# Kernel tuning notes

Measured on AMD Instinct MI355X. Metric: run time of the kernel, lower is better.

The kernel has to match this reference:

```python
import jax, jax.numpy as jnp
import numpy as np

C, T, H, W, K = 12, 10, 4, 7, 3  # hardcoded in the original forward
PAD = 1
EPS = 1e-5


def setup_inputs() -> dict:
    key = jax.random.key(0)
    ks = jax.random.split(key, 14)
    nt = 32768
    x = jax.random.normal(ks[0], (nt, C, T, H * W), jnp.float32)
    # G: Linear(T -> 2T) -> BN1d(2T) -> ReLU -> Linear(2T -> K) -> Softmax
    w_g1 = jax.random.normal(ks[1], (2 * T, T), jnp.float32) * 0.3
    g1_gamma = 1.0 + 0.1 * jax.random.normal(ks[2], (2 * T,), jnp.float32)
    g1_beta = 0.1 * jax.random.normal(ks[3], (2 * T,), jnp.float32)
    g1_mean = 0.1 * jax.random.normal(ks[4], (2 * T,), jnp.float32)
    g1_var = jax.random.uniform(ks[5], (2 * T,), jnp.float32, 0.5, 1.5)
    w_g2 = jax.random.normal(ks[6], (K, 2 * T), jnp.float32) * 0.3
    # L: Conv1d(C -> C//4, K) -> BN1d(C//4) -> ReLU -> Conv1d(C//4 -> C, 1) -> Sigmoid
    w_l1 = jax.random.normal(ks[7], (C // 4, C, K), jnp.float32) * 0.3
    l1_gamma = 1.0 + 0.1 * jax.random.normal(ks[8], (C // 4,), jnp.float32)
    l1_beta = 0.1 * jax.random.normal(ks[9], (C // 4,), jnp.float32)
    l1_mean = 0.1 * jax.random.normal(ks[10], (C // 4,), jnp.float32)
    l1_var = jax.random.uniform(ks[11], (C // 4,), jnp.float32, 0.5, 1.5)
    w_l2 = jax.random.normal(ks[12], (C, C // 4, 1), jnp.float32) * 0.3
    return dict(x=x, w_g1=w_g1, g1_gamma=g1_gamma, g1_beta=g1_beta,
                g1_mean=g1_mean, g1_var=g1_var, w_g2=w_g2, w_l1=w_l1,
                l1_gamma=l1_gamma, l1_beta=l1_beta, l1_mean=l1_mean,
                l1_var=l1_var, w_l2=w_l2)


def reference(x, w_g1, g1_gamma, g1_beta, g1_mean, g1_var, w_g2,
              w_l1, l1_gamma, l1_beta, l1_mean, l1_var, w_l2):
    n = x.shape[0]
    new_x = x.reshape(n, C, T, H, W)
    # adaptive_avg_pool2d((1,1)) == mean over spatial dims -> [n, C, T]
    pooled = new_x.mean(axis=(3, 4))
    # --- G branch: per-(sample,channel) temporal kernel, [n, C, K] ---
    rows = pooled.reshape(n * C, T)
    z = rows @ w_g1.T
    z = (z - g1_mean) * jax.lax.rsqrt(g1_var + EPS) * g1_gamma + g1_beta
    z = jax.nn.relu(z)
    kern = jax.nn.softmax(z @ w_g2.T, axis=-1).reshape(n, C, K)
    # --- L branch: local channel-temporal gating, [n, C, T] ---
    a = jax.lax.conv_general_dilated(pooled, w_l1, (1,), [(K // 2, K // 2)],
                                     dimension_numbers=('NCH', 'OIH', 'NCH'))
    a = (a - l1_mean[None, :, None]) * jax.lax.rsqrt(l1_var + EPS)[None, :, None] \
        * l1_gamma[None, :, None] + l1_beta[None, :, None]
    a = jax.nn.relu(a)
    a = jax.lax.conv_general_dilated(a, w_l2, (1,), [(0, 0)],
                                     dimension_numbers=('NCH', 'OIH', 'NCH'))
    act = jax.nn.sigmoid(a)  # [n, C, T]
    # --- modulate and apply per-(sample,channel) depthwise temporal conv ---
    xm = new_x * act[:, :, :, None, None]  # [n, C, T, H, W]
    xp = jnp.pad(xm, ((0, 0), (0, 0), (PAD, PAD), (0, 0), (0, 0)))
    out = kern[:, :, 0, None, None, None] * xp[:, :, 0:T]
    for j in range(1, K):  # K=3, tiny structural loop
        out = out + kern[:, :, j, None, None, None] * xp[:, :, j:j + T]
    # permute [n,c,t,h,w] -> [n,t,c,h,w] and flatten time into batch
    out = jnp.transpose(out, (0, 2, 1, 3, 4)).reshape(n * T, C, H, W)
    return out
```

## Files before the change

kernel.cpp:

```cpp
#include <hip/hip_runtime.h>


#define CC 12
#define TT 10
#define SAMPLE 3360
#define SAMPLE4 840
#define EPSF 1e-5f

typedef float f4 __attribute__((ext_vector_type(4)));

__global__ __launch_bounds__(128) void tam_kernel(
    const float* __restrict__ x,
    const float* __restrict__ w_g1,
    const float* __restrict__ g1_gamma, const float* __restrict__ g1_beta,
    const float* __restrict__ g1_mean,  const float* __restrict__ g1_var,
    const float* __restrict__ w_g2,
    const float* __restrict__ w_l1,
    const float* __restrict__ l1_gamma, const float* __restrict__ l1_beta,
    const float* __restrict__ l1_mean,  const float* __restrict__ l1_var,
    const float* __restrict__ w_l2,
    float* __restrict__ out)
{
    __shared__ f4    sx4[SAMPLE4];
    __shared__ float spool[120];
    __shared__ float sz[240];
    __shared__ float sa1[30];
    __shared__ float skern[36];

    const int n    = blockIdx.x;
    const int tid  = threadIdx.x;
    const int wid  = tid >> 6;
    const int lane = tid & 63;

    const f4* xg = reinterpret_cast<const f4*>(x + (size_t)n * SAMPLE);
    for (int i = wid; i < 13; i += 2) {
        __builtin_amdgcn_global_load_lds(
            (const __attribute__((address_space(1))) void*)(xg + i * 64 + lane),
            (__attribute__((address_space(3))) void*)(&sx4[i * 64]),
            16, 0, 0);
    }
    if (tid < 8) sx4[832 + tid] = xg[832 + tid];
    __syncthreads();

    if (tid < 120) {
        const f4* rp = sx4 + tid * 7;
        f4 a = rp[0];
        #pragma unroll
        for (int i = 1; i < 7; ++i) a += rp[i];
        spool[tid] = (a.x + a.y + a.z + a.w) * (1.0f / 28.0f);
    }
    __syncthreads();

    for (int task = tid; task < 270; task += 128) {
        if (task < 240) {
            const int c = task / 20, j = task % 20;
            float s = 0.f;
            #pragma unroll
            for (int t = 0; t < TT; ++t)
                s += spool[c * TT + t] * w_g1[j * TT + t];
            const float rs = rsqrtf(g1_var[j] + EPSF);
            sz[task] = fmaxf((s - g1_mean[j]) * rs * g1_gamma[j] + g1_beta[j], 0.f);
        } else {
            const int e = task - 240;
            const int m = e / TT, t = e % TT;
            float s = 0.f;
            #pragma unroll
            for (int c = 0; c < CC; ++c) {
                #pragma unroll
                for (int k = 0; k < 3; ++k) {
                    const int t2 = t + k - 1;
                    if (t2 >= 0 && t2 < TT)
                        s += spool[c * TT + t2] * w_l1[(m * CC + c) * 3 + k];
                }
            }
            const float rs = rsqrtf(l1_var[m] + EPSF);
            sa1[e] = fmaxf((s - l1_mean[m]) * rs * l1_gamma[m] + l1_beta[m], 0.f);
        }
    }
    __syncthreads();

    float* sact = spool;
    if (tid >= 116) {
        const int c = tid - 116;
        float sc0 = 0.f, sc1 = 0.f, sc2 = 0.f;
        #pragma unroll
        for (int j = 0; j < 20; ++j) {
            const float zj = sz[c * 20 + j];
            sc0 += zj * w_g2[j];
            sc1 += zj * w_g2[20 + j];
            sc2 += zj * w_g2[40 + j];
        }
        const float mx = fmaxf(sc0, fmaxf(sc1, sc2));
        const float e0 = __expf(sc0 - mx), e1 = __expf(sc1 - mx), e2 = __expf(sc2 - mx);
        const float ri = 1.0f / (e0 + e1 + e2);
        skern[c]      = e0 * ri;
        skern[12 + c] = e1 * ri;
        skern[24 + c] = e2 * ri;
    }
    if (tid < 120) {
        const int c = tid / TT, t = tid % TT;
        float s = 0.f;
        #pragma unroll
        for (int m = 0; m < 3; ++m) s += sa1[m * TT + t] * w_l2[c * 3 + m];
        sact[tid] = 1.0f / (1.0f + __expf(-s));
    }
    __syncthreads();

    f4* og = reinterpret_cast<f4*>(out + (size_t)n * SAMPLE);
    #pragma unroll
    for (int k = 0; k < 7; ++k) {
        const int v = tid + k * 128;
        if (k < 6 || tid < 72) {
            const int t   = v / 84;
            const int rem = v % 84;
            const int c   = rem / 7;
            const int s4  = rem % 7;
            const int base = c * 70 + s4;
            const float k0 = skern[c];
            const float k1 = skern[12 + c];
            const float k2 = skern[24 + c];
            f4 acc = (k1 * sact[c * TT + t]) * sx4[base + t * 7];
            if (t > 0)
                acc += (k0 * sact[c * TT + t - 1]) * sx4[base + (t - 1) * 7];
            if (t < TT - 1)
                acc += (k2 * sact[c * TT + t + 1]) * sx4[base + (t + 1) * 7];
            __builtin_nontemporal_store(acc, og + v);
        }
    }
}

extern "C" void kernel_launch(void* const* d_in, const int* in_sizes, int n_in,
                              void* d_out, int out_size, void* d_ws, size_t ws_size,
                              hipStream_t stream) {
    (void)n_in; (void)out_size; (void)d_ws; (void)ws_size;
    const float* x        = (const float*)d_in[0];
    const float* w_g1     = (const float*)d_in[1];
    const float* g1_gamma = (const float*)d_in[2];
    const float* g1_beta  = (const float*)d_in[3];
    const float* g1_mean  = (const float*)d_in[4];
    const float* g1_var   = (const float*)d_in[5];
    const float* w_g2     = (const float*)d_in[6];
    const float* w_l1     = (const float*)d_in[7];
    const float* l1_gamma = (const float*)d_in[8];
    const float* l1_beta  = (const float*)d_in[9];
    const float* l1_mean  = (const float*)d_in[10];
    const float* l1_var   = (const float*)d_in[11];
    const float* w_l2     = (const float*)d_in[12];
    float* out = (float*)d_out;

    const int n_total = in_sizes[0] / SAMPLE;
    tam_kernel<<<n_total, 128, 0, stream>>>(
        x, w_g1, g1_gamma, g1_beta, g1_mean, g1_var, w_g2,
        w_l1, l1_gamma, l1_beta, l1_mean, l1_var, w_l2, out);
}
```

Before: 193.6 us.

## Process two samples per 256-thread block with lightweight LDS barriers

Each block now loads two samples into separate LDS buffers up front with async global-to-LDS loads, then processes them sequentially with 256 threads. Syncs inside the per-sample pipeline are replaced by s_barrier plus an explicit lgkmcnt wait and sched barriers. The aim is to amortize block launch and barrier overhead and to keep more loads in flight per block. LDS per block doubles, which may reduce occupancy, and the second sample's load no longer overlaps with other blocks' compute. The grid assumes an even sample count.

```diff
diff --git a/kernel.cpp b/kernel.cpp
--- a/kernel.cpp
+++ b/kernel.cpp
@@ -9,7 +9,106 @@
 
 typedef float f4 __attribute__((ext_vector_type(4)));
 
-__global__ __launch_bounds__(128) void tam_kernel(
+#define FENCE() __builtin_amdgcn_sched_barrier(0)
+#define BLOCK_SYNC() do { asm volatile("s_waitcnt lgkmcnt(0)" ::: "memory"); \
+    FENCE(); __builtin_amdgcn_s_barrier(); FENCE(); } while (0)
+
+
+__device__ __forceinline__ void process_sample(
+    const f4* __restrict__ sx4, float* __restrict__ p,
+    const float* __restrict__ w_g1,
+    const float* __restrict__ g1_gamma, const float* __restrict__ g1_beta,
+    const float* __restrict__ g1_mean,  const float* __restrict__ g1_var,
+    const float* __restrict__ w_g2,
+    const float* __restrict__ w_l1,
+    const float* __restrict__ l1_gamma, const float* __restrict__ l1_beta,
+    const float* __restrict__ l1_mean,  const float* __restrict__ l1_var,
+    const float* __restrict__ w_l2,
+    f4* __restrict__ og, int tid)
+{
+    if (tid < 120) {
+        const f4* rp = sx4 + tid * 7;
+        f4 a = rp[0];
+        #pragma unroll
+        for (int i = 1; i < 7; ++i) a += rp[i];
+        p[tid] = (a.x + a.y + a.z + a.w) * (1.0f / 28.0f);
+    }
+    BLOCK_SYNC();
+
+    for (int task = tid; task < 270; task += 256) {
+        if (task < 240) {
+            const int c = task / 20, j = task % 20;
+            float s = 0.f;
+            #pragma unroll
+            for (int t = 0; t < TT; ++t)
+                s += p[c * TT + t] * w_g1[j * TT + t];
+            const float rs = rsqrtf(g1_var[j] + EPSF);
+            p[120 + task] = fmaxf((s - g1_mean[j]) * rs * g1_gamma[j] + g1_beta[j], 0.f);
+        } else {
+            const int e = task - 240;
+            const int m = e / TT, t = e % TT;
+            float s = 0.f;
+            #pragma unroll
+            for (int c = 0; c < CC; ++c) {
+                #pragma unroll
+                for (int k = 0; k < 3; ++k) {
+                    const int t2 = t + k - 1;
+                    if (t2 >= 0 && t2 < TT)
+                        s += p[c * TT + t2] * w_l1[(m * CC + c) * 3 + k];
+                }
+            }
+            const float rs = rsqrtf(l1_var[m] + EPSF);
+            p[360 + e] = fmaxf((s - l1_mean[m]) * rs * l1_gamma[m] + l1_beta[m], 0.f);
+        }
+    }
+    BLOCK_SYNC();
+
+    if (tid < CC) {
+        const int c = tid;
+        float sc0 = 0.f, sc1 = 0.f, sc2 = 0.f;
+        #pragma unroll
+        for (int j = 0; j < 20; ++j) {
+            const float zj = p[120 + c * 20 + j];
+            sc0 += zj * w_g2[j];
+            sc1 += zj * w_g2[20 + j];
+            sc2 += zj * w_g2[40 + j];
+        }
+        const float mx = fmaxf(sc0, fmaxf(sc1, sc2));
+        const float e0 = __expf(sc0 - mx), e1 = __expf(sc1 - mx), e2 = __expf(sc2 - mx);
+        const float ri = 1.0f / (e0 + e1 + e2);
+        p[390 + c] = e0 * ri;
+        p[402 + c] = e1 * ri;
+        p[414 + c] = e2 * ri;
+    }
+    if (tid >= 64 && tid < 64 + 120) {
+        const int idx = tid - 64;
+        const int c = idx / TT, t = idx % TT;
+        float s = 0.f;
+        #pragma unroll
+        for (int m = 0; m < 3; ++m) s += p[360 + m * TT + t] * w_l2[c * 3 + m];
+        p[idx] = 1.0f / (1.0f + __expf(-s));
+    }
+    BLOCK_SYNC();
+
+    for (int v = tid; v < SAMPLE4; v += 256) {
+        const int t   = v / 84;
+        const int rem = v % 84;
+        const int c   = rem / 7;
+        const int s4  = rem % 7;
+        const int base = c * 70 + s4;
+        const float k0 = p[390 + c];
+        const float k1 = p[402 + c];
+        const float k2 = p[414 + c];
+        f4 acc = (k1 * p[c * TT + t]) * sx4[base + t * 7];
+        if (t > 0)
+            acc += (k0 * p[c * TT + t - 1]) * sx4[base + (t - 1) * 7];
+        if (t < TT - 1)
+            acc += (k2 * p[c * TT + t + 1]) * sx4[base + (t + 1) * 7];
+        __builtin_nontemporal_store(acc, og + v);
+    }
+}
+
+__global__ __launch_bounds__(256) void tam_kernel(
     const float* __restrict__ x,
     const float* __restrict__ w_g1,
     const float* __restrict__ g1_gamma, const float* __restrict__ g1_beta,
@@ -21,112 +120,38 @@
     const float* __restrict__ w_l2,
     float* __restrict__ out)
 {
-    __shared__ f4    sx4[SAMPLE4];
-    __shared__ float spool[120];
-    __shared__ float sz[240];
-    __shared__ float sa1[30];
-    __shared__ float skern[36];
+    __shared__ f4    sxA[SAMPLE4], sxB[SAMPLE4];
+    __shared__ float scrA[426], scrB[426];
 
-    const int n    = blockIdx.x;
+    const int n0   = blockIdx.x * 2;
     const int tid  = threadIdx.x;
     const int wid  = tid >> 6;
     const int lane = tid & 63;
 
-    const f4* xg = reinterpret_cast<const f4*>(x + (size_t)n * SAMPLE);
-    for (int i = wid; i < 13; i += 2) {
+    const f4* xgA = reinterpret_cast<const f4*>(x + (size_t)n0 * SAMPLE);
+    const f4* xgB = reinterpret_cast<const f4*>(x + (size_t)(n0 + 1) * SAMPLE);
+    for (int i = wid; i < 13; i += 4) {
         __builtin_amdgcn_global_load_lds(
-            (const __attribute__((address_space(1))) void*)(xg + i * 64 + lane),
-            (__attribute__((address_space(3))) void*)(&sx4[i * 64]),
-            16, 0, 0);
+            (const __attribute__((address_space(1))) void*)(xgA + i * 64 + lane),
+            (__attribute__((address_space(3))) void*)(&sxA[i * 64]), 16, 0, 0);
+        __builtin_amdgcn_global_load_lds(
+            (const __attribute__((address_space(1))) void*)(xgB + i * 64 + lane),
+            (__attribute__((address_space(3))) void*)(&sxB[i * 64]), 16, 0, 0);
     }
-    if (tid < 8) sx4[832 + tid] = xg[832 + tid];
+    if (tid < 8)                sxA[832 + tid]     = xgA[832 + tid];
+    else if (tid < 16)          sxB[832 + tid - 8] = xgB[832 + tid - 8];
     __syncthreads();
 
-    if (tid < 120) {
-        const f4* rp = sx4 + tid * 7;
-        f4 a = rp[0];
-        #pragma unroll
-        for (int i = 1; i < 7; ++i) a += rp[i];
-        spool[tid] = (a.x + a.y + a.z + a.w) * (1.0f / 28.0f);
-    }
-    __syncthreads();
+    f4* ogA = reinterpret_cast<f4*>(out + (size_t)n0 * SAMPLE);
+    process_sample(sxA, scrA, w_g1, g1_gamma, g1_beta, g1_mean, g1_var,
+                   w_g2, w_l1, l1_gamma, l1_beta, l1_mean, l1_var, w_l2,
+                   ogA, tid);
+    BLOCK_SYNC();
 
-    for (int task = tid; task < 270; task += 128) {
-        if (task < 240) {
-            const int c = task / 20, j = task % 20;
-            float s = 0.f;
-            #pragma unroll
-            for (int t = 0; t < TT; ++t)
-                s += spool[c * TT + t] * w_g1[j * TT + t];
-            const float rs = rsqrtf(g1_var[j] + EPSF);
-            sz[task] = fmaxf((s - g1_mean[j]) * rs * g1_gamma[j] + g1_beta[j], 0.f);
-        } else {
-            const int e = task - 240;
-            const int m = e / TT, t = e % TT;
-            float s = 0.f;
-            #pragma unroll
-            for (int c = 0; c < CC; ++c) {
-                #pragma unroll
-                for (int k = 0; k < 3; ++k) {
-                    const int t2 = t + k - 1;
-                    if (t2 >= 0 && t2 < TT)
-                        s += spool[c * TT + t2] * w_l1[(m * CC + c) * 3 + k];
-                }
-            }
-            const float rs = rsqrtf(l1_var[m] + EPSF);
-            sa1[e] = fmaxf((s - l1_mean[m]) * rs * l1_gamma[m] + l1_beta[m], 0.f);
-        }
-    }
-    __syncthreads();
-
-    float* sact = spool;
-    if (tid >= 116) {
-        const int c = tid - 116;
-        float sc0 = 0.f, sc1 = 0.f, sc2 = 0.f;
-        #pragma unroll
-        for (int j = 0; j < 20; ++j) {
-            const float zj = sz[c * 20 + j];
-            sc0 += zj * w_g2[j];
-            sc1 += zj * w_g2[20 + j];
-            sc2 += zj * w_g2[40 + j];
-        }
-        const float mx = fmaxf(sc0, fmaxf(sc1, sc2));
-        const float e0 = __expf(sc0 - mx), e1 = __expf(sc1 - mx), e2 = __expf(sc2 - mx);
-        const float ri = 1.0f / (e0 + e1 + e2);
-        skern[c]      = e0 * ri;
-        skern[12 + c] = e1 * ri;
-        skern[24 + c] = e2 * ri;
-    }
-    if (tid < 120) {
-        const int c = tid / TT, t = tid % TT;
-        float s = 0.f;
-        #pragma unroll
-        for (int m = 0; m < 3; ++m) s += sa1[m * TT + t] * w_l2[c * 3 + m];
-        sact[tid] = 1.0f / (1.0f + __expf(-s));
-    }
-    __syncthreads();
-
-    f4* og = reinterpret_cast<f4*>(out + (size_t)n * SAMPLE);
-    #pragma unroll
-    for (int k = 0; k < 7; ++k) {
-        const int v = tid + k * 128;
-        if (k < 6 || tid < 72) {
-            const int t   = v / 84;
-            const int rem = v % 84;
-            const int c   = rem / 7;
-            const int s4  = rem % 7;
-            const int base = c * 70 + s4;
-            const float k0 = skern[c];
-            const float k1 = skern[12 + c];
-            const float k2 = skern[24 + c];
-            f4 acc = (k1 * sact[c * TT + t]) * sx4[base + t * 7];
-            if (t > 0)
-                acc += (k0 * sact[c * TT + t - 1]) * sx4[base + (t - 1) * 7];
-            if (t < TT - 1)
-                acc += (k2 * sact[c * TT + t + 1]) * sx4[base + (t + 1) * 7];
-            __builtin_nontemporal_store(acc, og + v);
-        }
-    }
+    f4* ogB = reinterpret_cast<f4*>(out + (size_t)(n0 + 1) * SAMPLE);
+    process_sample(sxB, scrB, w_g1, g1_gamma, g1_beta, g1_mean, g1_var,
+                   w_g2, w_l1, l1_gamma, l1_beta, l1_mean, l1_var, w_l2,
+                   ogB, tid);
 }
 
 extern "C" void kernel_launch(void* const* d_in, const int* in_sizes, int n_in,
@@ -149,7 +174,7 @@
     float* out = (float*)d_out;
 
     const int n_total = in_sizes[0] / SAMPLE;
-    tam_kernel<<<n_total, 128, 0, stream>>>(
+    tam_kernel<<<n_total / 2, 256, 0, stream>>>(
         x, w_g1, g1_gamma, g1_beta, g1_mean, g1_var, w_g2,
         w_l1, l1_gamma, l1_beta, l1_mean, l1_var, w_l2, out);
 }
```

Result: slower. 218.0 us (+12.6%).
